# Kernel tuning notes

Hardware: AMD Instinct MI355X
Metric: run time of the kernel (lower is better)

Reference implementation:

```python
import jax, jax.numpy as jnp
import numpy as np

B, T, F = 32, 2048, 64  # projection_dim must equal feature_dim for the original forward to type-check
SCALE = float(np.sqrt(F))


def setup_inputs() -> dict:
    key = jax.random.key(0)
    k_x, k_q, k_k = jax.random.split(key, 3)
    x = jax.random.normal(k_x, (B, T, F), dtype=jnp.float32)
    # torch nn.Linear weight is (out_features, in_features); y = x @ W.T
    lim = 1.0 / np.sqrt(F)
    W_q = jax.random.uniform(k_q, (F, F), dtype=jnp.float32, minval=-lim, maxval=lim)
    W_k = jax.random.uniform(k_k, (F, F), dtype=jnp.float32, minval=-lim, maxval=lim)
    gamma = jnp.zeros((1, 1, F), dtype=jnp.float32)
    return {"x": x, "W_q": W_q, "W_k": W_k, "gamma": gamma}


def reference(x, W_q, W_k, gamma):
    # Q, K: (B,T,F) -- Linear without bias: x @ W.T
    Q = jnp.einsum('btf,pf->btp', x, W_q)
    K = jnp.einsum('btf,pf->btp', x, W_k)
    # per-timestep outer product: scores[b,t,i,j] = Q[b,t,i]*K[b,t,j]/scale -> (B,T,F,F)
    scores = Q[..., :, None] * K[..., None, :] / SCALE
    attn_weights = jax.nn.softmax(scores, axis=-1)
    # mixed[b,t,i] = sum_j attn[b,t,i,j] * x[b,t,j]
    mixed = jnp.einsum('btij,btj->bti', attn_weights, x)
    out = x + gamma * mixed
    return (out, attn_weights)
```

## Files before the change

### kernel.cpp

```cpp
#include <hip/hip_runtime.h>


#define LOG2E 1.4426950408889634f

constexpr int F = 64;

__global__ __launch_bounds__(256, 2)
void fsattn(const float* __restrict__ X,
            const float* __restrict__ Wq,
            const float* __restrict__ Wk,
            const float* __restrict__ gamma,
            float* __restrict__ out,
            float* __restrict__ attn,
            int BT)
{
    const int lane = threadIdx.x & 63;
    const int wid  = threadIdx.x >> 6;
    const int gw   = (blockIdx.x << 2) + wid;
    const int nw   = gridDim.x << 2;

    __shared__ float x_lds[4][F];
    __shared__ float k_lds[4][F];

    float4 wq[16], wk[16];
#pragma unroll
    for (int i = 0; i < 16; ++i) {
        wq[i] = reinterpret_cast<const float4*>(Wq + lane * F)[i];
        wk[i] = reinterpret_cast<const float4*>(Wk + lane * F)[i];
    }
    const float g = gamma[lane];

    for (int t = gw; t < BT; t += nw) {
        const float xv = X[(size_t)t * F + lane];
        x_lds[wid][lane] = xv;
        __builtin_amdgcn_wave_barrier();

        float q = 0.f, k = 0.f;
#pragma unroll
        for (int i = 0; i < 16; ++i) {
            const float4 xb = reinterpret_cast<const float4*>(x_lds[wid])[i];
            q += wq[i].x * xb.x + wq[i].y * xb.y + wq[i].z * xb.z + wq[i].w * xb.w;
            k += wk[i].x * xb.x + wk[i].y * xb.y + wk[i].z * xb.z + wk[i].w * xb.w;
        }
        k_lds[wid][lane] = k;
        __builtin_amdgcn_wave_barrier();

        float kmax = k, kmin = k;
#pragma unroll
        for (int s = 1; s < 64; s <<= 1) {
            kmax = fmaxf(kmax, __shfl_xor(kmax, s, 64));
            kmin = fminf(kmin, __shfl_xor(kmin, s, 64));
        }

        const float qs = q * (0.125f * LOG2E);
        const float m  = fmaxf(qs * kmax, qs * kmin);

        float sum = 0.f, mix = 0.f;
#pragma unroll
        for (int j = 0; j < 16; ++j) {
            const float4 k4 = reinterpret_cast<const float4*>(k_lds[wid])[j];
            const float4 x4 = reinterpret_cast<const float4*>(x_lds[wid])[j];
            const float e0 = __builtin_amdgcn_exp2f(qs * k4.x - m);
            const float e1 = __builtin_amdgcn_exp2f(qs * k4.y - m);
            const float e2 = __builtin_amdgcn_exp2f(qs * k4.z - m);
            const float e3 = __builtin_amdgcn_exp2f(qs * k4.w - m);
            sum += (e0 + e1) + (e2 + e3);
            mix += e0 * x4.x + e1 * x4.y + e2 * x4.z + e3 * x4.w;
        }
        const float inv = __builtin_amdgcn_rcpf(sum);

        out[(size_t)t * F + lane] = xv + g * (mix * inv);

        float* ap = attn + (size_t)t * (F * F);
        const int sub = lane >> 4;
        const float4 kc = reinterpret_cast<const float4*>(k_lds[wid])[lane & 15];
#pragma unroll
        for (int i0 = 0; i0 < F; i0 += 4) {
            const int row = i0 + sub;
            const float qr = __shfl(qs, row, 64);
            const float ir = __shfl(inv, row, 64);
            const float mr = fmaxf(qr * kmax, qr * kmin);
            float4 w;
            w.x = __builtin_amdgcn_exp2f(qr * kc.x - mr) * ir;
            w.y = __builtin_amdgcn_exp2f(qr * kc.y - mr) * ir;
            w.z = __builtin_amdgcn_exp2f(qr * kc.z - mr) * ir;
            w.w = __builtin_amdgcn_exp2f(qr * kc.w - mr) * ir;
            reinterpret_cast<float4*>(ap + (size_t)row * F)[lane & 15] = w;
        }
    }
}

extern "C" void kernel_launch(void* const* d_in, const int* in_sizes, int n_in,
                              void* d_out, int out_size, void* d_ws, size_t ws_size,
                              hipStream_t stream) {
    const float* X     = (const float*)d_in[0];
    const float* Wq    = (const float*)d_in[1];
    const float* Wk    = (const float*)d_in[2];
    const float* gamma = (const float*)d_in[3];

    const int BT = in_sizes[0] / F;
    float* out  = (float*)d_out;
    float* attn = out + (size_t)BT * F;

    dim3 grid(1024), block(256);
    hipLaunchKernelGGL(fsattn, grid, block, 0, stream,
                       X, Wq, Wk, gamma, out, attn, BT);
}
```

Before: 238.2 us.

## Use fp16 dot2 projections, drop softmax max-shift, fold normalization into exp2

New measurement: 227.1 us. 4.7% less time.

```diff
diff --git a/kernel.cpp b/kernel.cpp
--- a/kernel.cpp
+++ b/kernel.cpp
@@ -5,7 +5,23 @@
 
 constexpr int F = 64;
 
-__global__ __launch_bounds__(256, 2)
+typedef _Float16 h2v __attribute__((ext_vector_type(2)));
+
+#if defined(__has_builtin)
+#if __has_builtin(__builtin_amdgcn_fdot2)
+#define HAVE_FDOT2 1
+#endif
+#endif
+
+static __device__ __forceinline__ float fdot2(h2v a, h2v b, float c) {
+#ifdef HAVE_FDOT2
+    return __builtin_amdgcn_fdot2(a, b, c, false);
+#else
+    return c + (float)a[0] * (float)b[0] + (float)a[1] * (float)b[1];
+#endif
+}
+
+__global__ __launch_bounds__(256, 4)
 void fsattn(const float* __restrict__ X,
             const float* __restrict__ Wq,
             const float* __restrict__ Wk,
@@ -19,73 +35,77 @@
     const int gw   = (blockIdx.x << 2) + wid;
     const int nw   = gridDim.x << 2;
 
-    __shared__ float x_lds[4][F];
-    __shared__ float k_lds[4][F];
+    __shared__ float    x_lds[4][F];
+    __shared__ float    k_lds[4][F];
+    __shared__ _Float16 xh_lds[4][F];
+    __shared__ float2   ql_lds[4][F];
 
-    float4 wq[16], wk[16];
+    h2v wq2[32], wk2[32];
 #pragma unroll
-    for (int i = 0; i < 16; ++i) {
-        wq[i] = reinterpret_cast<const float4*>(Wq + lane * F)[i];
-        wk[i] = reinterpret_cast<const float4*>(Wk + lane * F)[i];
+    for (int p = 0; p < 32; ++p) {
+        const float2 a = reinterpret_cast<const float2*>(Wq + lane * F)[p];
+        const float2 b = reinterpret_cast<const float2*>(Wk + lane * F)[p];
+        h2v ha; ha[0] = (_Float16)a.x; ha[1] = (_Float16)a.y;
+        h2v hb; hb[0] = (_Float16)b.x; hb[1] = (_Float16)b.y;
+        wq2[p] = ha; wk2[p] = hb;
     }
     const float g = gamma[lane];
 
     for (int t = gw; t < BT; t += nw) {
         const float xv = X[(size_t)t * F + lane];
-        x_lds[wid][lane] = xv;
+        x_lds[wid][lane]  = xv;
+        xh_lds[wid][lane] = (_Float16)xv;
         __builtin_amdgcn_wave_barrier();
 
         float q = 0.f, k = 0.f;
+        const h2v* xh = reinterpret_cast<const h2v*>(xh_lds[wid]);
 #pragma unroll
-        for (int i = 0; i < 16; ++i) {
-            const float4 xb = reinterpret_cast<const float4*>(x_lds[wid])[i];
-            q += wq[i].x * xb.x + wq[i].y * xb.y + wq[i].z * xb.z + wq[i].w * xb.w;
-            k += wk[i].x * xb.x + wk[i].y * xb.y + wk[i].z * xb.z + wk[i].w * xb.w;
+        for (int p = 0; p < 32; ++p) {
+            const h2v xp = xh[p];
+            q = fdot2(wq2[p], xp, q);
+            k = fdot2(wk2[p], xp, k);
         }
+        const float qs = q * (0.125f * LOG2E);
         k_lds[wid][lane] = k;
         __builtin_amdgcn_wave_barrier();
 
-        float kmax = k, kmin = k;
-#pragma unroll
-        for (int s = 1; s < 64; s <<= 1) {
-            kmax = fmaxf(kmax, __shfl_xor(kmax, s, 64));
-            kmin = fminf(kmin, __shfl_xor(kmin, s, 64));
-        }
-
-        const float qs = q * (0.125f * LOG2E);
-        const float m  = fmaxf(qs * kmax, qs * kmin);
-
-        float sum = 0.f, mix = 0.f;
+        float sum0 = 0.f, sum1 = 0.f, mix0 = 0.f, mix1 = 0.f;
 #pragma unroll
         for (int j = 0; j < 16; ++j) {
             const float4 k4 = reinterpret_cast<const float4*>(k_lds[wid])[j];
             const float4 x4 = reinterpret_cast<const float4*>(x_lds[wid])[j];
-            const float e0 = __builtin_amdgcn_exp2f(qs * k4.x - m);
-            const float e1 = __builtin_amdgcn_exp2f(qs * k4.y - m);
-            const float e2 = __builtin_amdgcn_exp2f(qs * k4.z - m);
-            const float e3 = __builtin_amdgcn_exp2f(qs * k4.w - m);
-            sum += (e0 + e1) + (e2 + e3);
-            mix += e0 * x4.x + e1 * x4.y + e2 * x4.z + e3 * x4.w;
+            const float e0 = __builtin_amdgcn_exp2f(qs * k4.x);
+            const float e1 = __builtin_amdgcn_exp2f(qs * k4.y);
+            const float e2 = __builtin_amdgcn_exp2f(qs * k4.z);
+            const float e3 = __builtin_amdgcn_exp2f(qs * k4.w);
+            sum0 += e0 + e1;
+            sum1 += e2 + e3;
+            mix0 = __builtin_fmaf(e0, x4.x, __builtin_fmaf(e1, x4.y, mix0));
+            mix1 = __builtin_fmaf(e2, x4.z, __builtin_fmaf(e3, x4.w, mix1));
         }
+        const float sum = sum0 + sum1;
         const float inv = __builtin_amdgcn_rcpf(sum);
+        const float li  = -__builtin_amdgcn_logf(sum);
+        float2 ql; ql.x = qs; ql.y = li;
+        ql_lds[wid][lane] = ql;
+        __builtin_amdgcn_wave_barrier();
 
-        out[(size_t)t * F + lane] = xv + g * (mix * inv);
+        out[(size_t)t * F + lane] = xv + g * ((mix0 + mix1) * inv);
 
         float* ap = attn + (size_t)t * (F * F);
         const int sub = lane >> 4;
-        const float4 kc = reinterpret_cast<const float4*>(k_lds[wid])[lane & 15];
+        const int c16 = lane & 15;
+        const float4 kc = reinterpret_cast<const float4*>(k_lds[wid])[c16];
 #pragma unroll
         for (int i0 = 0; i0 < F; i0 += 4) {
             const int row = i0 + sub;
-            const float qr = __shfl(qs, row, 64);
-            const float ir = __shfl(inv, row, 64);
-            const float mr = fmaxf(qr * kmax, qr * kmin);
+            const float2 qr = ql_lds[wid][row];
             float4 w;
-            w.x = __builtin_amdgcn_exp2f(qr * kc.x - mr) * ir;
-            w.y = __builtin_amdgcn_exp2f(qr * kc.y - mr) * ir;
-            w.z = __builtin_amdgcn_exp2f(qr * kc.z - mr) * ir;
-            w.w = __builtin_amdgcn_exp2f(qr * kc.w - mr) * ir;
-            reinterpret_cast<float4*>(ap + (size_t)row * F)[lane & 15] = w;
+            w.x = __builtin_amdgcn_exp2f(__builtin_fmaf(qr.x, kc.x, qr.y));
+            w.y = __builtin_amdgcn_exp2f(__builtin_fmaf(qr.x, kc.y, qr.y));
+            w.z = __builtin_amdgcn_exp2f(__builtin_fmaf(qr.x, kc.z, qr.y));
+            w.w = __builtin_amdgcn_exp2f(__builtin_fmaf(qr.x, kc.w, qr.y));
+            reinterpret_cast<float4*>(ap + (size_t)row * F)[c16] = w;
         }
     }
 }
```
